# Kernel tuning notes

Hardware: AMD Instinct MI355X
Metric: run time of the kernel (lower is better)

Reference implementation:

```python
import jax, jax.numpy as jnp
import numpy as np

N_NODES = 100000
N_EDGES = 3200000
IN_Z = 32
PROJ_H = 64
LOOP_D = 32
DEC_H = 64


def setup_inputs() -> dict:
    key = jax.random.key(0)
    ks = jax.random.split(key, 10)
    z_mod = jax.random.normal(ks[0], (N_NODES, IN_Z), dtype=jnp.float32)
    edge_index = jax.random.randint(ks[1], (2, N_EDGES), 0, N_NODES, dtype=jnp.int64)
    # loop_proj: Linear(32->64), ReLU, Linear(64->32)
    w1 = jax.random.normal(ks[2], (IN_Z, PROJ_H), dtype=jnp.float32) / np.sqrt(IN_Z)
    b1 = jnp.zeros((PROJ_H,), dtype=jnp.float32)
    w2 = jax.random.normal(ks[3], (PROJ_H, LOOP_D), dtype=jnp.float32) / np.sqrt(PROJ_H)
    b2 = jnp.zeros((LOOP_D,), dtype=jnp.float32)
    # decoder: Linear(2*loop_dim -> dec_hidden), ReLU, Linear(dec_hidden -> 1)
    dw1 = jax.random.normal(ks[4], (2 * LOOP_D, DEC_H), dtype=jnp.float32) / np.sqrt(2 * LOOP_D)
    db1 = jnp.zeros((DEC_H,), dtype=jnp.float32)
    dw2 = jax.random.normal(ks[5], (DEC_H, 1), dtype=jnp.float32) / np.sqrt(DEC_H)
    db2 = jnp.zeros((1,), dtype=jnp.float32)
    return {"z_mod": z_mod, "edge_index": edge_index, "w1": w1, "b1": b1,
            "w2": w2, "b2": b2, "dw1": dw1, "db1": db1, "dw2": dw2, "db2": db2}


def reference(z_mod, edge_index, w1, b1, w2, b2, dw1, db1, dw2, db2):
    # loop_proj: z_mod -> z_loop  [N, loop_dim]
    h = jax.nn.relu(z_mod @ w1 + b1)
    z_loop = h @ w2 + b2
    # edge-wise decoder: gather, concat, MLP
    zi = z_loop[edge_index[0]]            # [E, loop_dim]
    zj = z_loop[edge_index[1]]            # [E, loop_dim]
    he = jnp.concatenate([zi, zj], axis=-1)  # [E, 2*loop_dim]
    he = jax.nn.relu(he @ dw1 + db1)         # [E, dec_hidden]
    logits = (he @ dw2 + db2)[..., 0]        # [E]
    return logits
```

## Files before the change

kernel.cpp:

```cpp
#include <hip/hip_runtime.h>


typedef short bfrag4 __attribute__((ext_vector_type(4)));
typedef short s16x8  __attribute__((ext_vector_type(8)));
typedef float f32x4v __attribute__((ext_vector_type(4)));

#define N_NODES 100000
#define N_EDGES 3200000

__device__ __forceinline__ unsigned short f2bf(float f) {
    unsigned int i = __float_as_uint(f);
    unsigned int r = i + 0x7FFFu + ((i >> 16) & 1u);
    return (unsigned short)(r >> 16);
}

__device__ __forceinline__ bfrag4 cvt4(float x0, float x1, float x2, float x3) {
    bfrag4 v;
    v[0] = (short)f2bf(x0);
    v[1] = (short)f2bf(x1);
    v[2] = (short)f2bf(x2);
    v[3] = (short)f2bf(x3);
    return v;
}

__global__ __launch_bounds__(256) void node_proj_kernel(
    const float* __restrict__ z_mod,
    const float* __restrict__ w1,
    const float* __restrict__ b1,
    const float* __restrict__ w2,
    const float* __restrict__ b2,
    unsigned short* __restrict__ z_loop)
{
    __shared__ unsigned short hbuf[4][16 * 72];

    const int tid  = threadIdx.x;
    const int wave = tid >> 6;
    const int lane = tid & 63;
    const int quad = lane >> 4;
    const int col  = lane & 15;

    bfrag4 bw1[2][4];
    float  bias1[4];
    for (int t = 0; t < 4; ++t) {
        const int n = col + 16 * t;
        for (int s = 0; s < 2; ++s)
            for (int j = 0; j < 4; ++j)
                bw1[s][t][j] = (short)f2bf(w1[(s * 16 + quad * 4 + j) * 64 + n]);
        bias1[t] = b1[n];
    }
    bfrag4 bw2[4][2];
    float  bias2[2];
    for (int t = 0; t < 2; ++t) {
        const int n = col + 16 * t;
        for (int s = 0; s < 4; ++s)
            for (int j = 0; j < 4; ++j)
                bw2[s][t][j] = (short)f2bf(w2[(s * 16 + quad * 4 + j) * 32 + n]);
        bias2[t] = b2[n];
    }

    unsigned short* hrow = &hbuf[wave][0];

    const int gwave  = blockIdx.x * 4 + wave;
    const int nwaves = gridDim.x * 4;
    const int ntiles = N_NODES / 16;

    for (int tile = gwave; tile < ntiles; tile += nwaves) {
        const int node0 = tile * 16;
        const float* zrow = z_mod + (size_t)(node0 + col) * 32;

        f32x4v za0 = *(const f32x4v*)(zrow + 0 * 16 + quad * 4);
        f32x4v za1 = *(const f32x4v*)(zrow + 1 * 16 + quad * 4);
        bfrag4 a10 = cvt4(za0[0], za0[1], za0[2], za0[3]);
        bfrag4 a11 = cvt4(za1[0], za1[1], za1[2], za1[3]);

        f32x4v acc[4];
        for (int t = 0; t < 4; ++t) {
            f32x4v c = {bias1[t], bias1[t], bias1[t], bias1[t]};
            c = __builtin_amdgcn_mfma_f32_16x16x16bf16_1k(a10, bw1[0][t], c, 0, 0, 0);
            c = __builtin_amdgcn_mfma_f32_16x16x16bf16_1k(a11, bw1[1][t], c, 0, 0, 0);
            acc[t] = c;
        }

        for (int t = 0; t < 4; ++t)
            for (int r = 0; r < 4; ++r) {
                float v = acc[t][r];
                v = v > 0.f ? v : 0.f;
                hrow[(quad * 4 + r) * 72 + (col + 16 * t)] = f2bf(v);
            }
        asm volatile("" ::: "memory");

        f32x4v acc2[2];
        for (int t = 0; t < 2; ++t)
            acc2[t] = (f32x4v){bias2[t], bias2[t], bias2[t], bias2[t]};
        for (int s = 0; s < 4; ++s) {
            bfrag4 a2 = *(const bfrag4*)(hrow + col * 72 + s * 16 + quad * 4);
            for (int t = 0; t < 2; ++t)
                acc2[t] = __builtin_amdgcn_mfma_f32_16x16x16bf16_1k(a2, bw2[s][t], acc2[t], 0, 0, 0);
        }
        asm volatile("" ::: "memory");

        for (int t = 0; t < 2; ++t)
            for (int r = 0; r < 4; ++r)
                z_loop[(size_t)(node0 + quad * 4 + r) * 32 + (col + 16 * t)] =
                    f2bf(acc2[t][r]);
    }
}

__global__ __launch_bounds__(256) void edge_dec_kernel(
    const int*            __restrict__ eidx,
    const unsigned short* __restrict__ z_loop,
    const float*          __restrict__ dw1,
    const float*          __restrict__ db1,
    const float*          __restrict__ dw2,
    const float*          __restrict__ db2,
    float* __restrict__ out)
{
    const int tid  = threadIdx.x;
    const int lane = tid & 63;
    const int quad = lane >> 4;
    const int col  = lane & 15;

    s16x8 aw[2][4];
    float bias1[4][4];
    float w2v[4][4];
    for (int mt = 0; mt < 4; ++mt) {
        const int h = 16 * mt + col;
        for (int s = 0; s < 2; ++s)
            for (int j = 0; j < 8; ++j)
                aw[s][mt][j] = (short)f2bf(dw1[(32 * s + quad * 8 + j) * 64 + h]);
        for (int r = 0; r < 4; ++r) {
            bias1[mt][r] = db1[16 * mt + quad * 4 + r];
            w2v[mt][r]   = dw2[16 * mt + quad * 4 + r];
        }
    }
    const float bias2 = db2[0];

    const int gwave  = blockIdx.x * 4 + (tid >> 6);
    const int nwaves = gridDim.x * 4;
    const int npairs = N_EDGES / 32;

    for (int p = gwave; p < npairs; p += nwaves) {
        const int e0 = p * 32;

        const int srcA = eidx[e0 + col];
        const int srcB = eidx[e0 + 16 + col];
        const int dstA = eidx[N_EDGES + e0 + col];
        const int dstB = eidx[N_EDGES + e0 + 16 + col];

        s16x8 gA0 = *(const s16x8*)(z_loop + (size_t)srcA * 32 + quad * 8);
        s16x8 gA1 = *(const s16x8*)(z_loop + (size_t)dstA * 32 + quad * 8);
        s16x8 gB0 = *(const s16x8*)(z_loop + (size_t)srcB * 32 + quad * 8);
        s16x8 gB1 = *(const s16x8*)(z_loop + (size_t)dstB * 32 + quad * 8);

        f32x4v accA[4], accB[4];
        for (int mt = 0; mt < 4; ++mt) {
            f32x4v c = {bias1[mt][0], bias1[mt][1], bias1[mt][2], bias1[mt][3]};
            c = __builtin_amdgcn_mfma_f32_16x16x32_bf16(aw[0][mt], gA0, c, 0, 0, 0);
            c = __builtin_amdgcn_mfma_f32_16x16x32_bf16(aw[1][mt], gA1, c, 0, 0, 0);
            accA[mt] = c;
        }
        for (int mt = 0; mt < 4; ++mt) {
            f32x4v c = {bias1[mt][0], bias1[mt][1], bias1[mt][2], bias1[mt][3]};
            c = __builtin_amdgcn_mfma_f32_16x16x32_bf16(aw[0][mt], gB0, c, 0, 0, 0);
            c = __builtin_amdgcn_mfma_f32_16x16x32_bf16(aw[1][mt], gB1, c, 0, 0, 0);
            accB[mt] = c;
        }

        float pA = 0.f, pB = 0.f;
        for (int mt = 0; mt < 4; ++mt)
            for (int r = 0; r < 4; ++r) {
                float vA = accA[mt][r]; vA = vA > 0.f ? vA : 0.f;
                float vB = accB[mt][r]; vB = vB > 0.f ? vB : 0.f;
                pA += vA * w2v[mt][r];
                pB += vB * w2v[mt][r];
            }
        pA += __shfl_xor(pA, 16, 64);
        pA += __shfl_xor(pA, 32, 64);
        pB += __shfl_xor(pB, 16, 64);
        pB += __shfl_xor(pB, 32, 64);

        if (lane < 32) {
            float v = (lane < 16 ? pA : pB) + bias2;
            out[e0 + lane] = v;
        }
    }
}

extern "C" void kernel_launch(void* const* d_in, const int* in_sizes, int n_in,
                              void* d_out, int out_size, void* d_ws, size_t ws_size,
                              hipStream_t stream) {
    const float* z_mod = (const float*)d_in[0];
    const int*   eidx  = (const int*)d_in[1];
    const float* w1    = (const float*)d_in[2];
    const float* b1    = (const float*)d_in[3];
    const float* w2    = (const float*)d_in[4];
    const float* b2    = (const float*)d_in[5];
    const float* dw1   = (const float*)d_in[6];
    const float* db1   = (const float*)d_in[7];
    const float* dw2   = (const float*)d_in[8];
    const float* db2   = (const float*)d_in[9];
    float*          out    = (float*)d_out;
    unsigned short* z_loop = (unsigned short*)d_ws;

    node_proj_kernel<<<512, 256, 0, stream>>>(z_mod, w1, b1, w2, b2, z_loop);
    edge_dec_kernel<<<1536, 256, 0, stream>>>(eidx, z_loop, dw1, db1, dw2, db2, out);
}
```

Before: 161.1 us.

## Switch edge decoder to 32x32x16 MFMA tiles with prefetched edge indices

The edge decoder moves from 16x16x32 MFMA on two 16-edge halves to 32x32x16 MFMA, so one wave handles 32 edges in a single tile. This needs only one cross-lane shuffle instead of two per output and simplifies the final reduction. It also software-prefetches the next tile's src/dst indices while the current tile's gathers and MFMAs run, hiding index-load latency. The cost is larger accumulator register use (two f32x16) and a different weight fragment layout.

```diff
diff --git a/kernel.cpp b/kernel.cpp
--- a/kernel.cpp
+++ b/kernel.cpp
@@ -4,6 +4,7 @@
 typedef short bfrag4 __attribute__((ext_vector_type(4)));
 typedef short s16x8  __attribute__((ext_vector_type(8)));
 typedef float f32x4v __attribute__((ext_vector_type(4)));
+typedef float f32x16 __attribute__((ext_vector_type(16)));
 
 #define N_NODES 100000
 #define N_EDGES 3200000
@@ -115,74 +116,74 @@
     const float*          __restrict__ db2,
     float* __restrict__ out)
 {
-    const int tid  = threadIdx.x;
-    const int lane = tid & 63;
-    const int quad = lane >> 4;
-    const int col  = lane & 15;
-
-    s16x8 aw[2][4];
-    float bias1[4][4];
-    float w2v[4][4];
-    for (int mt = 0; mt < 4; ++mt) {
-        const int h = 16 * mt + col;
-        for (int s = 0; s < 2; ++s)
+    const int tid   = threadIdx.x;
+    const int lane  = tid & 63;
+    const int half  = lane >> 5;
+    const int col32 = lane & 31;
+
+    s16x8 aw[4][2];
+    f32x16 biasC[2];
+    float  w2v[2][16];
+    for (int mt = 0; mt < 2; ++mt) {
+        const int h = 32 * mt + col32;
+        for (int ks = 0; ks < 4; ++ks)
             for (int j = 0; j < 8; ++j)
-                aw[s][mt][j] = (short)f2bf(dw1[(32 * s + quad * 8 + j) * 64 + h]);
-        for (int r = 0; r < 4; ++r) {
-            bias1[mt][r] = db1[16 * mt + quad * 4 + r];
-            w2v[mt][r]   = dw2[16 * mt + quad * 4 + r];
+                aw[ks][mt][j] = (short)f2bf(dw1[(16 * ks + 8 * half + j) * 64 + h]);
+        for (int reg = 0; reg < 16; ++reg) {
+            const int row = (reg & 3) + 8 * (reg >> 2) + 4 * half;
+            biasC[mt][reg] = db1[32 * mt + row];
+            w2v[mt][reg]   = dw2[32 * mt + row];
         }
     }
     const float bias2 = db2[0];
 
     const int gwave  = blockIdx.x * 4 + (tid >> 6);
     const int nwaves = gridDim.x * 4;
-    const int npairs = N_EDGES / 32;
-
-    for (int p = gwave; p < npairs; p += nwaves) {
+    const int ntil   = N_EDGES / 32;
+
+    int sE = eidx[gwave * 32 + col32];
+    int dE = eidx[N_EDGES + gwave * 32 + col32];
+
+    for (int p = gwave; p < ntil; p += nwaves) {
         const int e0 = p * 32;
 
-        const int srcA = eidx[e0 + col];
-        const int srcB = eidx[e0 + 16 + col];
-        const int dstA = eidx[N_EDGES + e0 + col];
-        const int dstB = eidx[N_EDGES + e0 + 16 + col];
-
-        s16x8 gA0 = *(const s16x8*)(z_loop + (size_t)srcA * 32 + quad * 8);
-        s16x8 gA1 = *(const s16x8*)(z_loop + (size_t)dstA * 32 + quad * 8);
-        s16x8 gB0 = *(const s16x8*)(z_loop + (size_t)srcB * 32 + quad * 8);
-        s16x8 gB1 = *(const s16x8*)(z_loop + (size_t)dstB * 32 + quad * 8);
-
-        f32x4v accA[4], accB[4];
-        for (int mt = 0; mt < 4; ++mt) {
-            f32x4v c = {bias1[mt][0], bias1[mt][1], bias1[mt][2], bias1[mt][3]};
-            c = __builtin_amdgcn_mfma_f32_16x16x32_bf16(aw[0][mt], gA0, c, 0, 0, 0);
-            c = __builtin_amdgcn_mfma_f32_16x16x32_bf16(aw[1][mt], gA1, c, 0, 0, 0);
-            accA[mt] = c;
-        }
-        for (int mt = 0; mt < 4; ++mt) {
-            f32x4v c = {bias1[mt][0], bias1[mt][1], bias1[mt][2], bias1[mt][3]};
-            c = __builtin_amdgcn_mfma_f32_16x16x32_bf16(aw[0][mt], gB0, c, 0, 0, 0);
-            c = __builtin_amdgcn_mfma_f32_16x16x32_bf16(aw[1][mt], gB1, c, 0, 0, 0);
-            accB[mt] = c;
-        }
-
-        float pA = 0.f, pB = 0.f;
-        for (int mt = 0; mt < 4; ++mt)
-            for (int r = 0; r < 4; ++r) {
-                float vA = accA[mt][r]; vA = vA > 0.f ? vA : 0.f;
-                float vB = accB[mt][r]; vB = vB > 0.f ? vB : 0.f;
-                pA += vA * w2v[mt][r];
-                pB += vB * w2v[mt][r];
-            }
-        pA += __shfl_xor(pA, 16, 64);
-        pA += __shfl_xor(pA, 32, 64);
-        pB += __shfl_xor(pB, 16, 64);
-        pB += __shfl_xor(pB, 32, 64);
-
-        if (lane < 32) {
-            float v = (lane < 16 ? pA : pB) + bias2;
-            out[e0 + lane] = v;
-        }
+        const unsigned short* zs = z_loop + (size_t)sE * 32 + half * 8;
+        const unsigned short* zd = z_loop + (size_t)dE * 32 + half * 8;
+        s16x8 g0a = *(const s16x8*)(zs);
+        s16x8 g0b = *(const s16x8*)(zs + 16);
+        s16x8 g1a = *(const s16x8*)(zd);
+        s16x8 g1b = *(const s16x8*)(zd + 16);
+
+        const int pn = p + nwaves;
+        const int pc = pn < ntil ? pn : gwave;
+        sE = eidx[pc * 32 + col32];
+        dE = eidx[N_EDGES + pc * 32 + col32];
+
+        f32x16 acc0, acc1;
+        {
+            f32x16 c = __builtin_amdgcn_mfma_f32_32x32x16_bf16(aw[0][0], g0a, biasC[0], 0, 0, 0);
+            c = __builtin_amdgcn_mfma_f32_32x32x16_bf16(aw[1][0], g0b, c, 0, 0, 0);
+            c = __builtin_amdgcn_mfma_f32_32x32x16_bf16(aw[2][0], g1a, c, 0, 0, 0);
+            acc0 = __builtin_amdgcn_mfma_f32_32x32x16_bf16(aw[3][0], g1b, c, 0, 0, 0);
+        }
+        {
+            f32x16 c = __builtin_amdgcn_mfma_f32_32x32x16_bf16(aw[0][1], g0a, biasC[1], 0, 0, 0);
+            c = __builtin_amdgcn_mfma_f32_32x32x16_bf16(aw[1][1], g0b, c, 0, 0, 0);
+            c = __builtin_amdgcn_mfma_f32_32x32x16_bf16(aw[2][1], g1a, c, 0, 0, 0);
+            acc1 = __builtin_amdgcn_mfma_f32_32x32x16_bf16(aw[3][1], g1b, c, 0, 0, 0);
+        }
+
+        float pv = 0.f;
+        for (int reg = 0; reg < 16; ++reg) {
+            float v0 = acc0[reg]; v0 = v0 > 0.f ? v0 : 0.f;
+            float v1 = acc1[reg]; v1 = v1 > 0.f ? v1 : 0.f;
+            pv += v0 * w2v[0][reg];
+            pv += v1 * w2v[1][reg];
+        }
+        pv += __shfl_xor(pv, 32, 64);
+
+        if (lane < 32)
+            out[e0 + lane] = pv + bias2;
     }
 }
 
```

Measured after the change: 152.7 us. 1.05x faster.
